# Kernel tuning notes

Hardware: AMD Instinct MI355X
Metric: run time of the kernel (lower is better)

The kernel has to match this reference:

```python
import jax, jax.numpy as jnp
import numpy as np

N = 8192
IN_DIM, HID_DIM, OUT_DIM = 32, 64, 16


def setup_inputs() -> dict:
    key = jax.random.key(0)
    k1, k2, k3, k4, k5, k6, k7 = jax.random.split(key, 7)
    s1 = 1.0 / np.sqrt(IN_DIM)
    s2 = 1.0 / np.sqrt(HID_DIM)
    return {
        "adj1": jax.random.normal(k1, (N, N), jnp.float32),
        "adj2": jax.random.normal(k2, (N, N), jnp.float32),
        "features": jax.random.normal(k3, (N, IN_DIM), jnp.float32),
        # gc1 linear (shared across both aggregation branches)
        "W1": jax.random.uniform(k4, (IN_DIM, HID_DIM), jnp.float32, -s1, s1),
        "b1": jax.random.uniform(k5, (HID_DIM,), jnp.float32, -s1, s1),
        # gc2 linear
        "W2": jax.random.uniform(k6, (HID_DIM, OUT_DIM), jnp.float32, -s2, s2),
        "b2": jax.random.uniform(k7, (OUT_DIM,), jnp.float32, -s2, s2),
    }


def _gc_layer(adj1, adj2, x, W, b):
    # branch 1: aggregate -> shared linear -> relu
    o1 = jax.nn.relu(jnp.matmul(adj1, x) @ W + b)
    # branch 2: same linear weights
    o2 = jax.nn.relu(jnp.matmul(adj2, x) @ W + b)
    return o1 + o2


def reference(adj1, adj2, features, W1, b1, W2, b2):
    h1 = _gc_layer(adj1, adj2, features, W1, b1)  # [N, HID_DIM]
    h2 = _gc_layer(adj1, adj2, h1, W2, b2)        # [N, OUT_DIM]
    return h2
```

## Files before the change

### kernel.cpp

```cpp
#include <hip/hip_runtime.h>
#include <stdint.h>

#define NN 8192
#define IN_DIM 32
#define HID_DIM 64
#define OUT_DIM 16

typedef __attribute__((ext_vector_type(8))) short short8;
typedef __attribute__((ext_vector_type(4))) float f32x4;

__device__ __forceinline__ short f2bf_bits(float x){
  uint32_t u = __builtin_bit_cast(uint32_t, x);
  u += 0x7FFFu + ((u >> 16) & 1u);
  return (short)(u >> 16);
}

__device__ __forceinline__ short8 cvt8(f32x4 lo, f32x4 hi){
  short8 r;
  r[0]=f2bf_bits(lo[0]); r[1]=f2bf_bits(lo[1]); r[2]=f2bf_bits(lo[2]); r[3]=f2bf_bits(lo[3]);
  r[4]=f2bf_bits(hi[0]); r[5]=f2bf_bits(hi[1]); r[6]=f2bf_bits(hi[2]); r[7]=f2bf_bits(hi[3]);
  return r;
}

__global__ __launch_bounds__(256) void prep_xt(const float* __restrict__ X, short* __restrict__ Xt){
  int i = blockIdx.x * 256 + threadIdx.x;
  int r = i >> 5, c = i & 31;
  Xt[(size_t)c * NN + r] = f2bf_bits(X[i]);
}

__global__ __launch_bounds__(256, 4) void gcn_mm1(const float* __restrict__ adj1, const float* __restrict__ adj2,
                                                  const short* __restrict__ Xt,
                                                  float* __restrict__ Y1p, float* __restrict__ Y2p, int klen){
  const int lane = threadIdx.x & 63;
  const int wave = threadIdx.x >> 6;
  const int bm   = blockIdx.x;
  const int ks   = blockIdx.y;
  const int arow = bm * 64 + wave * 16 + (lane & 15);
  const int kgrp = (lane >> 4) * 8;
  const int k0   = ks * klen;

  const float* a1  = adj1 + (size_t)arow * NN + k0 + kgrp;
  const float* a2  = adj2 + (size_t)arow * NN + k0 + kgrp;
  const short* bp0 = Xt + (size_t)(lane & 15) * NN + k0 + kgrp;
  const short* bp1 = bp0 + (size_t)16 * NN;

  f32x4 acc10 = {0.f,0.f,0.f,0.f}, acc11 = {0.f,0.f,0.f,0.f};
  f32x4 acc20 = {0.f,0.f,0.f,0.f}, acc21 = {0.f,0.f,0.f,0.f};

  const int nsteps = klen >> 5;

  f32x4 A1l = *(const f32x4*)(a1), A1h = *(const f32x4*)(a1 + 4);
  f32x4 A2l = *(const f32x4*)(a2), A2h = *(const f32x4*)(a2 + 4);
  short8 B0 = *(const short8*)(bp0), B1 = *(const short8*)(bp1);

  #pragma unroll 1
  for (int t = 0; t < nsteps - 1; ++t){
    a1 += 32; a2 += 32; bp0 += 32; bp1 += 32;
    f32x4 nA1l = *(const f32x4*)(a1), nA1h = *(const f32x4*)(a1 + 4);
    f32x4 nA2l = *(const f32x4*)(a2), nA2h = *(const f32x4*)(a2 + 4);
    short8 nB0 = *(const short8*)(bp0), nB1 = *(const short8*)(bp1);
    short8 fa1 = cvt8(A1l, A1h);
    short8 fa2 = cvt8(A2l, A2h);
    acc10 = __builtin_amdgcn_mfma_f32_16x16x32_bf16(fa1, B0, acc10, 0, 0, 0);
    acc11 = __builtin_amdgcn_mfma_f32_16x16x32_bf16(fa1, B1, acc11, 0, 0, 0);
    acc20 = __builtin_amdgcn_mfma_f32_16x16x32_bf16(fa2, B0, acc20, 0, 0, 0);
    acc21 = __builtin_amdgcn_mfma_f32_16x16x32_bf16(fa2, B1, acc21, 0, 0, 0);
    A1l = nA1l; A1h = nA1h; A2l = nA2l; A2h = nA2h; B0 = nB0; B1 = nB1;
  }
  {
    short8 fa1 = cvt8(A1l, A1h);
    short8 fa2 = cvt8(A2l, A2h);
    acc10 = __builtin_amdgcn_mfma_f32_16x16x32_bf16(fa1, B0, acc10, 0, 0, 0);
    acc11 = __builtin_amdgcn_mfma_f32_16x16x32_bf16(fa1, B1, acc11, 0, 0, 0);
    acc20 = __builtin_amdgcn_mfma_f32_16x16x32_bf16(fa2, B0, acc20, 0, 0, 0);
    acc21 = __builtin_amdgcn_mfma_f32_16x16x32_bf16(fa2, B1, acc21, 0, 0, 0);
  }

  const int orow = bm * 64 + wave * 16 + (lane >> 4) * 4;
  const int col  = lane & 15;
  float* y1 = Y1p + ((size_t)ks * NN + orow) * IN_DIM + col;
  float* y2 = Y2p + ((size_t)ks * NN + orow) * IN_DIM + col;
  #pragma unroll
  for (int r = 0; r < 4; ++r){
    y1[(size_t)r * IN_DIM]      = acc10[r];
    y1[(size_t)r * IN_DIM + 16] = acc11[r];
    y2[(size_t)r * IN_DIM]      = acc20[r];
    y2[(size_t)r * IN_DIM + 16] = acc21[r];
  }
}

__global__ __launch_bounds__(256) void l1_combine(const float* __restrict__ Y1p, const float* __restrict__ Y2p,
                                                  const float* __restrict__ W1, const float* __restrict__ b1,
                                                  short* __restrict__ H1t, int S){
  __shared__ float sW[IN_DIM * HID_DIM];
  __shared__ float sb[HID_DIM];
  __shared__ float sy[4][2][IN_DIM];
  const int tid = threadIdx.x;
  for (int i = tid; i < IN_DIM * HID_DIM; i += 256) sW[i] = W1[i];
  if (tid < HID_DIM) sb[tid] = b1[tid];
  const int sub = tid >> 6, t = tid & 63;
  const int row = blockIdx.x * 4 + sub;
  {
    const int br = t >> 5, c = t & 31;
    const float* P = br ? Y2p : Y1p;
    float s = 0.f;
    for (int sp = 0; sp < S; ++sp) s += P[((size_t)sp * NN + row) * IN_DIM + c];
    sy[sub][br][c] = s;
  }
  __syncthreads();
  float h1v = sb[t], h2v = sb[t];
  #pragma unroll
  for (int k = 0; k < IN_DIM; ++k){
    h1v += sy[sub][0][k] * sW[k * HID_DIM + t];
    h2v += sy[sub][1][k] * sW[k * HID_DIM + t];
  }
  float h = fmaxf(h1v, 0.f) + fmaxf(h2v, 0.f);
  H1t[(size_t)t * NN + row] = f2bf_bits(h);
}

__global__ __launch_bounds__(256, 4) void gcn_mm2(const float* __restrict__ adj1, const float* __restrict__ adj2,
                                                  const short* __restrict__ H1t,
                                                  float* __restrict__ Z1p, float* __restrict__ Z2p, int klen){
  const int lane = threadIdx.x & 63;
  const int wave = threadIdx.x >> 6;
  const int bm   = gridDim.x - 1 - blockIdx.x;
  const int ks   = gridDim.y - 1 - blockIdx.y;
  const int arow = bm * 64 + wave * 16 + (lane & 15);
  const int kgrp = (lane >> 4) * 8;
  const int nsteps = klen >> 5;
  const int klast  = ks * klen + (nsteps - 1) * 32;

  const float* a1 = adj1 + (size_t)arow * NN + klast + kgrp;
  const float* a2 = adj2 + (size_t)arow * NN + klast + kgrp;
  const short* bp[4];
  #pragma unroll
  for (int f = 0; f < 4; ++f)
    bp[f] = H1t + (size_t)(f * 16 + (lane & 15)) * NN + klast + kgrp;

  f32x4 acc1[4] = {{0.f,0.f,0.f,0.f},{0.f,0.f,0.f,0.f},{0.f,0.f,0.f,0.f},{0.f,0.f,0.f,0.f}};
  f32x4 acc2[4] = {{0.f,0.f,0.f,0.f},{0.f,0.f,0.f,0.f},{0.f,0.f,0.f,0.f},{0.f,0.f,0.f,0.f}};

  f32x4 A1l = *(const f32x4*)(a1), A1h = *(const f32x4*)(a1 + 4);
  f32x4 A2l = *(const f32x4*)(a2), A2h = *(const f32x4*)(a2 + 4);
  short8 B[4];
  #pragma unroll
  for (int f = 0; f < 4; ++f) B[f] = *(const short8*)(bp[f]);

  #pragma unroll 1
  for (int t = 0; t < nsteps - 1; ++t){
    a1 -= 32; a2 -= 32;
    #pragma unroll
    for (int f = 0; f < 4; ++f) bp[f] -= 32;
    f32x4 nA1l = *(const f32x4*)(a1), nA1h = *(const f32x4*)(a1 + 4);
    f32x4 nA2l = *(const f32x4*)(a2), nA2h = *(const f32x4*)(a2 + 4);
    short8 nB[4];
    #pragma unroll
    for (int f = 0; f < 4; ++f) nB[f] = *(const short8*)(bp[f]);
    short8 fa1 = cvt8(A1l, A1h);
    short8 fa2 = cvt8(A2l, A2h);
    #pragma unroll
    for (int f = 0; f < 4; ++f){
      acc1[f] = __builtin_amdgcn_mfma_f32_16x16x32_bf16(fa1, B[f], acc1[f], 0, 0, 0);
      acc2[f] = __builtin_amdgcn_mfma_f32_16x16x32_bf16(fa2, B[f], acc2[f], 0, 0, 0);
    }
    A1l = nA1l; A1h = nA1h; A2l = nA2l; A2h = nA2h;
    #pragma unroll
    for (int f = 0; f < 4; ++f) B[f] = nB[f];
  }
  {
    short8 fa1 = cvt8(A1l, A1h);
    short8 fa2 = cvt8(A2l, A2h);
    #pragma unroll
    for (int f = 0; f < 4; ++f){
      acc1[f] = __builtin_amdgcn_mfma_f32_16x16x32_bf16(fa1, B[f], acc1[f], 0, 0, 0);
      acc2[f] = __builtin_amdgcn_mfma_f32_16x16x32_bf16(fa2, B[f], acc2[f], 0, 0, 0);
    }
  }

  const int orow = bm * 64 + wave * 16 + (lane >> 4) * 4;
  const int col  = lane & 15;
  float* z1 = Z1p + ((size_t)ks * NN + orow) * HID_DIM + col;
  float* z2 = Z2p + ((size_t)ks * NN + orow) * HID_DIM + col;
  #pragma unroll
  for (int r = 0; r < 4; ++r){
    #pragma unroll
    for (int f = 0; f < 4; ++f){
      z1[(size_t)r * HID_DIM + f * 16] = acc1[f][r];
      z2[(size_t)r * HID_DIM + f * 16] = acc2[f][r];
    }
  }
}

__global__ __launch_bounds__(256) void l2_combine(const float* __restrict__ Z1p, const float* __restrict__ Z2p,
                                                  const float* __restrict__ W2, const float* __restrict__ b2,
                                                  float* __restrict__ out, int S){
  __shared__ float sW[HID_DIM * OUT_DIM];
  __shared__ float sb[OUT_DIM];
  __shared__ float sz[4][2][HID_DIM];
  const int tid = threadIdx.x;
  for (int i = tid; i < HID_DIM * OUT_DIM; i += 256) sW[i] = W2[i];
  if (tid < OUT_DIM) sb[tid] = b2[tid];
  const int sub = tid >> 6, t = tid & 63;
  const int row = blockIdx.x * 4 + sub;
  float s1 = 0.f, s2 = 0.f;
  for (int sp = 0; sp < S; ++sp){
    s1 += Z1p[((size_t)sp * NN + row) * HID_DIM + t];
    s2 += Z2p[((size_t)sp * NN + row) * HID_DIM + t];
  }
  sz[sub][0][t] = s1;
  sz[sub][1][t] = s2;
  __syncthreads();
  if (t < OUT_DIM){
    float a = sb[t], b = sb[t];
    #pragma unroll
    for (int k = 0; k < HID_DIM; ++k){
      a += sz[sub][0][k] * sW[k * OUT_DIM + t];
      b += sz[sub][1][k] * sW[k * OUT_DIM + t];
    }
    out[(size_t)row * OUT_DIM + t] = fmaxf(a, 0.f) + fmaxf(b, 0.f);
  }
}

extern "C" void kernel_launch(void* const* d_in, const int* in_sizes, int n_in,
                              void* d_out, int out_size, void* d_ws, size_t ws_size,
                              hipStream_t stream){
  const float* adj1 = (const float*)d_in[0];
  const float* adj2 = (const float*)d_in[1];
  const float* X    = (const float*)d_in[2];
  const float* W1   = (const float*)d_in[3];
  const float* b1   = (const float*)d_in[4];
  const float* W2   = (const float*)d_in[5];
  const float* b2   = (const float*)d_in[6];
  float* out = (float*)d_out;

  char* ws = (char*)d_ws;
  short* Xt  = (short*)ws;
  short* H1t = (short*)(ws + (size_t)512 * 1024);
  size_t off = (size_t)1536 * 1024;

  int S = 8;
  while (S > 1 && off + (size_t)S * 6 * 1024 * 1024 > ws_size) S >>= 1;
  float* Y1p = (float*)(ws + off);
  float* Y2p = Y1p + (size_t)S * NN * IN_DIM;
  float* Z1p = Y2p + (size_t)S * NN * IN_DIM;
  float* Z2p = Z1p + (size_t)S * NN * HID_DIM;
  const int klen = NN / S;

  prep_xt  <<<dim3(NN * IN_DIM / 256), dim3(256), 0, stream>>>(X, Xt);
  gcn_mm1  <<<dim3(NN / 64, S), dim3(256), 0, stream>>>(adj1, adj2, Xt, Y1p, Y2p, klen);
  l1_combine<<<dim3(NN / 4), dim3(256), 0, stream>>>(Y1p, Y2p, W1, b1, H1t, S);
  gcn_mm2  <<<dim3(NN / 64, S), dim3(256), 0, stream>>>(adj1, adj2, H1t, Z1p, Z2p, klen);
  l2_combine<<<dim3(NN / 4), dim3(256), 0, stream>>>(Z1p, Z2p, W2, b2, out, S);
}
```

Before: 284.8 us.

## Apply W1 before adjacency aggregation and share partial buffers across layers

The first layer now computes X@W1 up front (reassociating (adj@X)@W1 as adj@(X@W1)), so the first adjacency matmul produces 64 output columns instead of 32. The layer-1 combine reduces to a sum plus bias and relu. The partial-sum buffers are shared between both matmul passes, which shrinks the workspace. Both passes are bound by reading the fp32 adjacency matrices, so the extra MFMA and B-operand traffic in the first pass could cost some time. The real gain is simpler glue and lower workspace use.

```diff
diff --git a/kernel.cpp b/kernel.cpp
--- a/kernel.cpp
+++ b/kernel.cpp
@@ -22,15 +22,25 @@
   return r;
 }
 
-__global__ __launch_bounds__(256) void prep_xt(const float* __restrict__ X, short* __restrict__ Xt){
-  int i = blockIdx.x * 256 + threadIdx.x;
-  int r = i >> 5, c = i & 31;
-  Xt[(size_t)c * NN + r] = f2bf_bits(X[i]);
-}
-
-__global__ __launch_bounds__(256, 4) void gcn_mm1(const float* __restrict__ adj1, const float* __restrict__ adj2,
-                                                  const short* __restrict__ Xt,
-                                                  float* __restrict__ Y1p, float* __restrict__ Y2p, int klen){
+__global__ __launch_bounds__(256) void k_g(const float* __restrict__ X, const float* __restrict__ W1,
+                                           short* __restrict__ Gt){
+  const int b    = blockIdx.x;
+  const int rb   = (b & 127) * 64;
+  const int cg   = b >> 7;
+  const int lane = threadIdx.x & 63;
+  const int c    = cg * 4 + (threadIdx.x >> 6);
+  const int r    = rb + lane;
+  const float* xr = X + (size_t)r * IN_DIM;
+  float acc = 0.f;
+  #pragma unroll
+  for (int k = 0; k < IN_DIM; ++k)
+    acc += xr[k] * W1[(size_t)k * HID_DIM + c];
+  Gt[(size_t)c * NN + r] = f2bf_bits(acc);
+}
+
+__global__ __launch_bounds__(256, 4) void mm_fwd(const float* __restrict__ adj1, const float* __restrict__ adj2,
+                                                 const short* __restrict__ Bt,
+                                                 float* __restrict__ P1, float* __restrict__ P2, int klen){
   const int lane = threadIdx.x & 63;
   const int wave = threadIdx.x >> 6;
   const int bm   = blockIdx.x;
@@ -39,88 +49,71 @@
   const int kgrp = (lane >> 4) * 8;
   const int k0   = ks * klen;
 
-  const float* a1  = adj1 + (size_t)arow * NN + k0 + kgrp;
-  const float* a2  = adj2 + (size_t)arow * NN + k0 + kgrp;
-  const short* bp0 = Xt + (size_t)(lane & 15) * NN + k0 + kgrp;
-  const short* bp1 = bp0 + (size_t)16 * NN;
-
-  f32x4 acc10 = {0.f,0.f,0.f,0.f}, acc11 = {0.f,0.f,0.f,0.f};
-  f32x4 acc20 = {0.f,0.f,0.f,0.f}, acc21 = {0.f,0.f,0.f,0.f};
+  const float* a1 = adj1 + (size_t)arow * NN + k0 + kgrp;
+  const float* a2 = adj2 + (size_t)arow * NN + k0 + kgrp;
+  const short* bp[4];
+  #pragma unroll
+  for (int f = 0; f < 4; ++f)
+    bp[f] = Bt + (size_t)(f * 16 + (lane & 15)) * NN + k0 + kgrp;
+
+  f32x4 acc1[4] = {{0.f,0.f,0.f,0.f},{0.f,0.f,0.f,0.f},{0.f,0.f,0.f,0.f},{0.f,0.f,0.f,0.f}};
+  f32x4 acc2[4] = {{0.f,0.f,0.f,0.f},{0.f,0.f,0.f,0.f},{0.f,0.f,0.f,0.f},{0.f,0.f,0.f,0.f}};
 
   const int nsteps = klen >> 5;
-
   f32x4 A1l = *(const f32x4*)(a1), A1h = *(const f32x4*)(a1 + 4);
   f32x4 A2l = *(const f32x4*)(a2), A2h = *(const f32x4*)(a2 + 4);
-  short8 B0 = *(const short8*)(bp0), B1 = *(const short8*)(bp1);
+  short8 B[4];
+  #pragma unroll
+  for (int f = 0; f < 4; ++f) B[f] = *(const short8*)(bp[f]);
 
   #pragma unroll 1
   for (int t = 0; t < nsteps - 1; ++t){
-    a1 += 32; a2 += 32; bp0 += 32; bp1 += 32;
+    a1 += 32; a2 += 32;
+    #pragma unroll
+    for (int f = 0; f < 4; ++f) bp[f] += 32;
     f32x4 nA1l = *(const f32x4*)(a1), nA1h = *(const f32x4*)(a1 + 4);
     f32x4 nA2l = *(const f32x4*)(a2), nA2h = *(const f32x4*)(a2 + 4);
-    short8 nB0 = *(const short8*)(bp0), nB1 = *(const short8*)(bp1);
-    short8 fa1 = cvt8(A1l, A1h);
-    short8 fa2 = cvt8(A2l, A2h);
-    acc10 = __builtin_amdgcn_mfma_f32_16x16x32_bf16(fa1, B0, acc10, 0, 0, 0);
-    acc11 = __builtin_amdgcn_mfma_f32_16x16x32_bf16(fa1, B1, acc11, 0, 0, 0);
-    acc20 = __builtin_amdgcn_mfma_f32_16x16x32_bf16(fa2, B0, acc20, 0, 0, 0);
-    acc21 = __builtin_amdgcn_mfma_f32_16x16x32_bf16(fa2, B1, acc21, 0, 0, 0);
-    A1l = nA1l; A1h = nA1h; A2l = nA2l; A2h = nA2h; B0 = nB0; B1 = nB1;
+    short8 nB[4];
+    #pragma unroll
+    for (int f = 0; f < 4; ++f) nB[f] = *(const short8*)(bp[f]);
+    short8 fa1 = cvt8(A1l, A1h);
+    short8 fa2 = cvt8(A2l, A2h);
+    #pragma unroll
+    for (int f = 0; f < 4; ++f){
+      acc1[f] = __builtin_amdgcn_mfma_f32_16x16x32_bf16(fa1, B[f], acc1[f], 0, 0, 0);
+      acc2[f] = __builtin_amdgcn_mfma_f32_16x16x32_bf16(fa2, B[f], acc2[f], 0, 0, 0);
+    }
+    A1l = nA1l; A1h = nA1h; A2l = nA2l; A2h = nA2h;
+    #pragma unroll
+    for (int f = 0; f < 4; ++f) B[f] = nB[f];
   }
   {
     short8 fa1 = cvt8(A1l, A1h);
     short8 fa2 = cvt8(A2l, A2h);
-    acc10 = __builtin_amdgcn_mfma_f32_16x16x32_bf16(fa1, B0, acc10, 0, 0, 0);
-    acc11 = __builtin_amdgcn_mfma_f32_16x16x32_bf16(fa1, B1, acc11, 0, 0, 0);
-    acc20 = __builtin_amdgcn_mfma_f32_16x16x32_bf16(fa2, B0, acc20, 0, 0, 0);
-    acc21 = __builtin_amdgcn_mfma_f32_16x16x32_bf16(fa2, B1, acc21, 0, 0, 0);
+    #pragma unroll
+    for (int f = 0; f < 4; ++f){
+      acc1[f] = __builtin_amdgcn_mfma_f32_16x16x32_bf16(fa1, B[f], acc1[f], 0, 0, 0);
+      acc2[f] = __builtin_amdgcn_mfma_f32_16x16x32_bf16(fa2, B[f], acc2[f], 0, 0, 0);
+    }
   }
 
   const int orow = bm * 64 + wave * 16 + (lane >> 4) * 4;
   const int col  = lane & 15;
-  float* y1 = Y1p + ((size_t)ks * NN + orow) * IN_DIM + col;
-  float* y2 = Y2p + ((size_t)ks * NN + orow) * IN_DIM + col;
+  float* p1 = P1 + ((size_t)ks * NN + orow) * HID_DIM + col;
+  float* p2 = P2 + ((size_t)ks * NN + orow) * HID_DIM + col;
   #pragma unroll
   for (int r = 0; r < 4; ++r){
-    y1[(size_t)r * IN_DIM]      = acc10[r];
-    y1[(size_t)r * IN_DIM + 16] = acc11[r];
-    y2[(size_t)r * IN_DIM]      = acc20[r];
-    y2[(size_t)r * IN_DIM + 16] = acc21[r];
-  }
-}
-
-__global__ __launch_bounds__(256) void l1_combine(const float* __restrict__ Y1p, const float* __restrict__ Y2p,
-                                                  const float* __restrict__ W1, const float* __restrict__ b1,
-                                                  short* __restrict__ H1t, int S){
-  __shared__ float sW[IN_DIM * HID_DIM];
-  __shared__ float sb[HID_DIM];
-  __shared__ float sy[4][2][IN_DIM];
-  const int tid = threadIdx.x;
-  for (int i = tid; i < IN_DIM * HID_DIM; i += 256) sW[i] = W1[i];
-  if (tid < HID_DIM) sb[tid] = b1[tid];
-  const int sub = tid >> 6, t = tid & 63;
-  const int row = blockIdx.x * 4 + sub;
-  {
-    const int br = t >> 5, c = t & 31;
-    const float* P = br ? Y2p : Y1p;
-    float s = 0.f;
-    for (int sp = 0; sp < S; ++sp) s += P[((size_t)sp * NN + row) * IN_DIM + c];
-    sy[sub][br][c] = s;
-  }
-  __syncthreads();
-  float h1v = sb[t], h2v = sb[t];
-  #pragma unroll
-  for (int k = 0; k < IN_DIM; ++k){
-    h1v += sy[sub][0][k] * sW[k * HID_DIM + t];
-    h2v += sy[sub][1][k] * sW[k * HID_DIM + t];
-  }
-  float h = fmaxf(h1v, 0.f) + fmaxf(h2v, 0.f);
-  H1t[(size_t)t * NN + row] = f2bf_bits(h);
-}
-
-__global__ __launch_bounds__(256, 4) void gcn_mm2(const float* __restrict__ adj1, const float* __restrict__ adj2,
-                                                  const short* __restrict__ H1t,
-                                                  float* __restrict__ Z1p, float* __restrict__ Z2p, int klen){
+    #pragma unroll
+    for (int f = 0; f < 4; ++f){
+      p1[(size_t)r * HID_DIM + f * 16] = acc1[f][r];
+      p2[(size_t)r * HID_DIM + f * 16] = acc2[f][r];
+    }
+  }
+}
+
+__global__ __launch_bounds__(256, 4) void mm_rev(const float* __restrict__ adj1, const float* __restrict__ adj2,
+                                                 const short* __restrict__ Bt,
+                                                 float* __restrict__ P1, float* __restrict__ P2, int klen){
   const int lane = threadIdx.x & 63;
   const int wave = threadIdx.x >> 6;
   const int bm   = gridDim.x - 1 - blockIdx.x;
@@ -135,7 +128,7 @@
   const short* bp[4];
   #pragma unroll
   for (int f = 0; f < 4; ++f)
-    bp[f] = H1t + (size_t)(f * 16 + (lane & 15)) * NN + klast + kgrp;
+    bp[f] = Bt + (size_t)(f * 16 + (lane & 15)) * NN + klast + kgrp;
 
   f32x4 acc1[4] = {{0.f,0.f,0.f,0.f},{0.f,0.f,0.f,0.f},{0.f,0.f,0.f,0.f},{0.f,0.f,0.f,0.f}};
   f32x4 acc2[4] = {{0.f,0.f,0.f,0.f},{0.f,0.f,0.f,0.f},{0.f,0.f,0.f,0.f},{0.f,0.f,0.f,0.f}};
@@ -179,16 +172,32 @@
 
   const int orow = bm * 64 + wave * 16 + (lane >> 4) * 4;
   const int col  = lane & 15;
-  float* z1 = Z1p + ((size_t)ks * NN + orow) * HID_DIM + col;
-  float* z2 = Z2p + ((size_t)ks * NN + orow) * HID_DIM + col;
+  float* p1 = P1 + ((size_t)ks * NN + orow) * HID_DIM + col;
+  float* p2 = P2 + ((size_t)ks * NN + orow) * HID_DIM + col;
   #pragma unroll
   for (int r = 0; r < 4; ++r){
     #pragma unroll
     for (int f = 0; f < 4; ++f){
-      z1[(size_t)r * HID_DIM + f * 16] = acc1[f][r];
-      z2[(size_t)r * HID_DIM + f * 16] = acc2[f][r];
-    }
-  }
+      p1[(size_t)r * HID_DIM + f * 16] = acc1[f][r];
+      p2[(size_t)r * HID_DIM + f * 16] = acc2[f][r];
+    }
+  }
+}
+
+__global__ __launch_bounds__(256) void l1_combine(const float* __restrict__ Y1p, const float* __restrict__ Y2p,
+                                                  const float* __restrict__ b1,
+                                                  short* __restrict__ H1t, int S){
+  const int lane = threadIdx.x & 63;
+  const int wave = threadIdx.x >> 6;
+  const int row  = blockIdx.x * 4 + wave;
+  float s1 = 0.f, s2 = 0.f;
+  for (int sp = 0; sp < S; ++sp){
+    s1 += Y1p[((size_t)sp * NN + row) * HID_DIM + lane];
+    s2 += Y2p[((size_t)sp * NN + row) * HID_DIM + lane];
+  }
+  const float b = b1[lane];
+  float h = fmaxf(s1 + b, 0.f) + fmaxf(s2 + b, 0.f);
+  H1t[(size_t)lane * NN + row] = f2bf_bits(h);
 }
 
 __global__ __launch_bounds__(256) void l2_combine(const float* __restrict__ Z1p, const float* __restrict__ Z2p,
@@ -234,21 +243,19 @@
   float* out = (float*)d_out;
 
   char* ws = (char*)d_ws;
-  short* Xt  = (short*)ws;
-  short* H1t = (short*)(ws + (size_t)512 * 1024);
-  size_t off = (size_t)1536 * 1024;
+  short* Gt  = (short*)ws;
+  short* H1t = (short*)(ws + (size_t)1024 * 1024);
+  const size_t off = (size_t)2 * 1024 * 1024;
 
   int S = 8;
-  while (S > 1 && off + (size_t)S * 6 * 1024 * 1024 > ws_size) S >>= 1;
-  float* Y1p = (float*)(ws + off);
-  float* Y2p = Y1p + (size_t)S * NN * IN_DIM;
-  float* Z1p = Y2p + (size_t)S * NN * IN_DIM;
-  float* Z2p = Z1p + (size_t)S * NN * HID_DIM;
+  while (S > 1 && off + (size_t)S * 4 * 1024 * 1024 > ws_size) S >>= 1;
+  float* P1 = (float*)(ws + off);
+  float* P2 = P1 + (size_t)S * NN * HID_DIM;
   const int klen = NN / S;
 
-  prep_xt  <<<dim3(NN * IN_DIM / 256), dim3(256), 0, stream>>>(X, Xt);
-  gcn_mm1  <<<dim3(NN / 64, S), dim3(256), 0, stream>>>(adj1, adj2, Xt, Y1p, Y2p, klen);
-  l1_combine<<<dim3(NN / 4), dim3(256), 0, stream>>>(Y1p, Y2p, W1, b1, H1t, S);
-  gcn_mm2  <<<dim3(NN / 64, S), dim3(256), 0, stream>>>(adj1, adj2, H1t, Z1p, Z2p, klen);
-  l2_combine<<<dim3(NN / 4), dim3(256), 0, stream>>>(Z1p, Z2p, W2, b2, out, S);
-}
+  k_g      <<<dim3(2048),       dim3(256), 0, stream>>>(X, W1, Gt);
+  mm_fwd   <<<dim3(NN / 64, S), dim3(256), 0, stream>>>(adj1, adj2, Gt, P1, P2, klen);
+  l1_combine<<<dim3(NN / 4),    dim3(256), 0, stream>>>(P1, P2, b1, H1t, S);
+  mm_rev   <<<dim3(NN / 64, S), dim3(256), 0, stream>>>(adj1, adj2, H1t, P1, P2, klen);
+  l2_combine<<<dim3(NN / 4),    dim3(256), 0, stream>>>(P1, P2, W2, b2, out, S);
+}
```

Measured after the change: 356.4 us. 25.2% more time.
